# Optimization experiments

Measured on AMD Instinct MI355X. Metric: run time of the kernel, lower is better.

Reference implementation:

```python
import jax, jax.numpy as jnp
import numpy as np
from itertools import combinations_with_replacement

INPUT_DIM = 128
DEGREE = 2

# Static index arrays for degree-2 terms (i<=j), matching
# combinations_with_replacement order.
_pairs = np.array(list(combinations_with_replacement(range(INPUT_DIM), DEGREE)), dtype=np.int32)
I_IDX = jnp.asarray(_pairs[:, 0])  # [d*(d+1)/2]
J_IDX = jnp.asarray(_pairs[:, 1])


def setup_inputs() -> dict:
    key = jax.random.key(0)
    k1, k2, k3 = jax.random.split(key, 3)
    B, D, N = 8192, INPUT_DIM, 512
    num_outputs = D + D * (D + 1) // 2  # 8384
    x = jax.random.normal(k1, (B, D), dtype=jnp.float32)
    weights = jax.random.normal(k2, (N, num_outputs), dtype=jnp.float32)
    bias = jax.random.normal(k3, (N,), dtype=jnp.float32)
    return {"x": x, "weights": weights, "bias": bias}


def reference(x, weights, bias):
    # Polynomial feature expansion: [x, x_i * x_j for i<=j]
    poly = x[:, I_IDX] * x[:, J_IDX]          # [B, d*(d+1)/2]
    feats = jnp.concatenate([x, poly], axis=1)  # [B, num_outputs]
    # (output.unsqueeze(1) * weights.unsqueeze(0)).sum(-1) == feats @ weights.T
    return jnp.einsum('bo,no->bn', feats, weights) + bias
```

## Files before the change

kernel.cpp:

```cpp
#include <hip/hip_runtime.h>
#include <hip/hip_bf16.h>
#include <stdint.h>

#define D_IN   128
#define NPOLY  8256
#define KDIM   8384
#define B_ROWS 8192
#define N_COLS 512

#define WBF_OFF   0
#define WBF_BYTES ((size_t)N_COLS * KDIM * 2)
#define FEA_OFF   WBF_BYTES
#define FEA_BYTES ((size_t)B_ROWS * KDIM * 2)
#define WS_NEED   (FEA_OFF + FEA_BYTES)

typedef __attribute__((ext_vector_type(8))) short    bf16x8_t;
typedef __attribute__((ext_vector_type(8))) float    f32x8_t;
typedef __attribute__((ext_vector_type(4))) float    f32x4_t;
typedef __attribute__((ext_vector_type(4))) uint32_t u32x4_t;

__device__ __forceinline__ uint32_t pk2(float lo, float hi) {
  uint32_t r;
  asm("v_cvt_pk_bf16_f32 %0, %1, %2" : "=v"(r) : "v"(lo), "v"(hi));
  return r;
}

__device__ __forceinline__ void async_load16(void* lds_dst, const void* g_src) {
  __builtin_amdgcn_global_load_lds(
      (const __attribute__((address_space(1))) void*)g_src,
      (__attribute__((address_space(3))) void*)lds_dst,
      16, 0, 0);
}

#define NB_FEAT 4096
#define NB_INIT 4096
#define NB_WCNV 2096
__global__ __launch_bounds__(256) void fused_prep(
    const float* __restrict__ x, const float* __restrict__ w,
    const float* __restrict__ bias, float* __restrict__ out,
    uint16_t* __restrict__ wb, uint16_t* __restrict__ feats) {
  __shared__ float xs[2][D_IN];
  __shared__ __align__(16) uint16_t pr[2][KDIM];
  const int blk = blockIdx.x;
  const int tid = threadIdx.x;

  if (blk < NB_FEAT) {
    const int r0 = blk * 2;
    xs[tid >> 7][tid & 127] = x[(size_t)r0 * D_IN + tid];
    __syncthreads();
    if (tid < 32) {
      int row = tid >> 4, c8 = (tid & 15) * 8;
      u32x4_t o;
#pragma unroll
      for (int h = 0; h < 4; ++h)
        o[h] = pk2(xs[row][c8 + 2 * h], xs[row][c8 + 2 * h + 1]);
      *(u32x4_t*)&pr[row][c8] = o;
    }
    for (int it = 0; it < 5; ++it) {
      int g = tid + it * 256;
      if (g >= NPOLY / 8) break;
      int p0 = 8 * g;
      float t = 66049.0f - 8.0f * (float)p0;
      int i = (int)((257.0f - sqrtf(t)) * 0.5f);
      while (i > 0 && (i * (257 - i)) / 2 > p0) --i;
      while (i < 127 && ((i + 1) * (257 - (i + 1))) / 2 <= p0) ++i;
      int j = i + (p0 - (i * (257 - i)) / 2);
      float xi0 = xs[0][i], xi1 = xs[1][i];
      float q0[8], q1[8];
#pragma unroll
      for (int e = 0; e < 8; ++e) {
        q0[e] = xi0 * xs[0][j];
        q1[e] = xi1 * xs[1][j];
        if (e < 7) {
          if (j == 127) { ++i; j = i; xi0 = xs[0][i]; xi1 = xs[1][i]; }
          else ++j;
        }
      }
      u32x4_t o0, o1;
#pragma unroll
      for (int h = 0; h < 4; ++h) {
        o0[h] = pk2(q0[2 * h], q0[2 * h + 1]);
        o1[h] = pk2(q1[2 * h], q1[2 * h + 1]);
      }
      *(u32x4_t*)&pr[0][D_IN + p0] = o0;
      *(u32x4_t*)&pr[1][D_IN + p0] = o1;
    }
    __syncthreads();
    uint16_t* d0 = feats + (size_t)r0 * KDIM;
    for (int q = tid; q < 2 * (KDIM / 8); q += 256) {
      int row = (q >= KDIM / 8);
      int g = q - (row ? KDIM / 8 : 0);
      *(bf16x8_t*)(d0 + (size_t)row * KDIM + g * 8) =
          *(const bf16x8_t*)&pr[row][g * 8];
    }
  } else if (blk < NB_FEAT + NB_INIT) {
    int idx = (blk - NB_FEAT) * 256 + tid;
    f32x4_t bv = *(const f32x4_t*)(bias + ((idx * 4) & (N_COLS - 1)));
    *(f32x4_t*)(out + (size_t)idx * 4) = bv;
  } else {
    int g = (blk - NB_FEAT - NB_INIT) * 256 + tid;
    f32x8_t v = *(const f32x8_t*)(w + (size_t)g * 8);
    u32x4_t o;
#pragma unroll
    for (int h = 0; h < 4; ++h) o[h] = pk2(v[2 * h], v[2 * h + 1]);
    *(u32x4_t*)(wb + (size_t)g * 8) = o;
  }
}

#define BMT 128
#define BNT 128
#define BKT 64
#define KSTEPS 131
#define KCUT 66

__global__ __launch_bounds__(256, 2) void gemm_poly(
    const uint16_t* __restrict__ A,
    const uint16_t* __restrict__ W,
    float* __restrict__ out) {
  __shared__ __align__(16) uint16_t sA[BMT * BKT];
  __shared__ __align__(16) uint16_t sW[BNT * BKT];

  const int tid  = threadIdx.x;
  const int lane = tid & 63;
  const int wv   = tid >> 6;
  const int wr   = wv >> 1;
  const int wc   = wv & 1;
  const int hi   = lane >> 4;
  const int lr   = lane & 15;

  const int b0 = blockIdx.x * BMT;
  const int n0 = blockIdx.y * BNT;
  const int kt0 = (blockIdx.z == 0) ? 0 : KCUT;
  const int kt1 = (blockIdx.z == 0) ? KCUT : KSTEPS;

  int rowq[4], cbxq[4];
#pragma unroll
  for (int q = 0; q < 4; ++q) {
    int L = q * 4096 + tid * 16;
    int row = L >> 7;
    int cb  = L & 127;
    rowq[q] = row;
    cbxq[q] = cb ^ ((row & 7) << 4);
  }

  int offA[4][2], offW[4][2];
#pragma unroll
  for (int f = 0; f < 4; ++f) {
    int rowA = wr * 64 + f * 16 + lr;
    int rowW = wc * 64 + f * 16 + lr;
#pragma unroll
    for (int kh = 0; kh < 2; ++kh) {
      int kb = kh * 64 + hi * 16;
      offA[f][kh] = rowA * 128 + (kb ^ ((rowA & 7) << 4));
      offW[f][kh] = rowW * 128 + (kb ^ ((rowW & 7) << 4));
    }
  }

  f32x4_t acc[4][4];
#pragma unroll
  for (int mf = 0; mf < 4; ++mf)
#pragma unroll
    for (int nf = 0; nf < 4; ++nf) {
      f32x4_t z = {0.f, 0.f, 0.f, 0.f};
      acc[mf][nf] = z;
    }

  const char* Ab = (const char*)A;
  const char* Wb = (const char*)W;

#define STAGE(kt)                                                              \
  {                                                                            \
    _Pragma("unroll")                                                          \
    for (int q = 0; q < 4; ++q) {                                              \
      const char* srcA =                                                       \
          Ab + ((size_t)(b0 + rowq[q]) * KDIM + (kt) * BKT) * 2 + cbxq[q];     \
      async_load16((char*)sA + q * 4096 + tid * 16, srcA);                     \
    }                                                                          \
    _Pragma("unroll")                                                          \
    for (int q = 0; q < 4; ++q) {                                              \
      const char* srcW =                                                       \
          Wb + ((size_t)(n0 + rowq[q]) * KDIM + (kt) * BKT) * 2 + cbxq[q];     \
      async_load16((char*)sW + q * 4096 + tid * 16, srcW);                     \
    }                                                                          \
  }

  STAGE(kt0);
  for (int kt = kt0; kt < kt1; ++kt) {
    __syncthreads();
    bf16x8_t a[4][2], b[4][2];
#pragma unroll
    for (int mf = 0; mf < 4; ++mf)
#pragma unroll
      for (int kh = 0; kh < 2; ++kh)
        a[mf][kh] = *(const bf16x8_t*)((const char*)sA + offA[mf][kh]);
#pragma unroll
    for (int nf = 0; nf < 4; ++nf)
#pragma unroll
      for (int kh = 0; kh < 2; ++kh)
        b[nf][kh] = *(const bf16x8_t*)((const char*)sW + offW[nf][kh]);
#pragma unroll
    for (int mf = 0; mf < 4; ++mf)
#pragma unroll
      for (int nf = 0; nf < 4; ++nf) {
        acc[mf][nf] = __builtin_amdgcn_mfma_f32_16x16x32_bf16(
            a[mf][0], b[nf][0], acc[mf][nf], 0, 0, 0);
        acc[mf][nf] = __builtin_amdgcn_mfma_f32_16x16x32_bf16(
            a[mf][1], b[nf][1], acc[mf][nf], 0, 0, 0);
      }
    __syncthreads();
    if (kt + 1 < kt1) STAGE(kt + 1);
  }

#pragma unroll
  for (int mf = 0; mf < 4; ++mf) {
    int row = b0 + wr * 64 + mf * 16 + hi * 4;
#pragma unroll
    for (int nf = 0; nf < 4; ++nf) {
      int col = n0 + wc * 64 + nf * 16 + lr;
#pragma unroll
      for (int r = 0; r < 4; ++r) {
        atomicAdd(&out[(size_t)(row + r) * N_COLS + col], acc[mf][nf][r]);
      }
    }
  }
#undef STAGE
}

__global__ void naive_poly(const float* __restrict__ x, const float* __restrict__ w,
                           const float* __restrict__ bias, float* __restrict__ out) {
  size_t o = (size_t)blockIdx.x * 256 + threadIdx.x;
  if (o >= (size_t)B_ROWS * N_COLS) return;
  int n = (int)(o >> 13);
  int b = (int)(o & (B_ROWS - 1));
  const float* xr = x + (size_t)b * D_IN;
  const float* wr = w + (size_t)n * KDIM;
  float acc = bias[n];
  for (int k = 0; k < D_IN; ++k) acc += wr[k] * xr[k];
  int p = D_IN;
  for (int i = 0; i < D_IN; ++i) {
    float xi = xr[i];
    for (int j = i; j < D_IN; ++j) acc += wr[p++] * xi * xr[j];
  }
  out[(size_t)b * N_COLS + n] = acc;
}

extern "C" void kernel_launch(void* const* d_in, const int* in_sizes, int n_in,
                              void* d_out, int out_size, void* d_ws, size_t ws_size,
                              hipStream_t stream) {
  const float* x    = (const float*)d_in[0];
  const float* w    = (const float*)d_in[1];
  const float* bias = (const float*)d_in[2];
  float* out = (float*)d_out;

  if (ws_size < WS_NEED) {
    naive_poly<<<(B_ROWS * N_COLS) / 256, 256, 0, stream>>>(x, w, bias, out);
    return;
  }

  char* ws = (char*)d_ws;
  uint16_t* wb  = (uint16_t*)(ws + WBF_OFF);
  uint16_t* fe  = (uint16_t*)(ws + FEA_OFF);

  fused_prep<<<NB_FEAT + NB_INIT + NB_WCNV, 256, 0, stream>>>(x, w, bias, out, wb, fe);
  gemm_poly<<<dim3(B_ROWS / BMT, N_COLS / BNT, 2), 256, 0, stream>>>(fe, wb, out);
}
```

Baseline: 200.6 us.

## Double-buffer A in LDS, load W straight to registers, remap blocks for XCD locality

The GEMM now double-buffers the A tile in LDS and prefetches the next step's A while computing the current one, using explicit vmcnt waits and raw barriers. The W operand is loaded straight from global memory into registers, ping-ponging between two register sets, so its LDS staging goes away. The launch becomes a 1D grid whose block index is remapped so that blocks on the same XCD share tiles, and MFMA sections run at raised wave priority. The risks are higher register pressure from the register-held W and uncoalesced per-lane global loads for W. A clamp is also added in the feature index computation.

After: 268.3 us. 1.34x slower.

```diff
diff --git a/kernel.cpp b/kernel.cpp
--- a/kernel.cpp
+++ b/kernel.cpp
@@ -62,6 +62,7 @@
       int p0 = 8 * g;
       float t = 66049.0f - 8.0f * (float)p0;
       int i = (int)((257.0f - sqrtf(t)) * 0.5f);
+      if (i < 0) i = 0; if (i > 127) i = 127;
       while (i > 0 && (i * (257 - i)) / 2 > p0) --i;
       while (i < 127 && ((i + 1) * (257 - (i + 1))) / 2 <= p0) ++i;
       int j = i + (p0 - (i * (257 - i)) / 2);
@@ -117,8 +118,7 @@
     const uint16_t* __restrict__ A,
     const uint16_t* __restrict__ W,
     float* __restrict__ out) {
-  __shared__ __align__(16) uint16_t sA[BMT * BKT];
-  __shared__ __align__(16) uint16_t sW[BNT * BKT];
+  __shared__ __align__(16) uint16_t sA[2 * BMT * BKT];
 
   const int tid  = threadIdx.x;
   const int lane = tid & 63;
@@ -128,10 +128,17 @@
   const int hi   = lane >> 4;
   const int lr   = lane & 15;
 
-  const int b0 = blockIdx.x * BMT;
-  const int n0 = blockIdx.y * BNT;
-  const int kt0 = (blockIdx.z == 0) ? 0 : KCUT;
-  const int kt1 = (blockIdx.z == 0) ? KCUT : KSTEPS;
+  const int bid = blockIdx.x;
+  const int lin = (bid & 7) * 64 + (bid >> 3);
+  const int bz  = lin >> 8;
+  const int rem = lin & 255;
+  const int by  = rem >> 6;
+  const int bx  = rem & 63;
+
+  const int b0  = bx * BMT;
+  const int n0  = by * BNT;
+  const int kt0 = (bz == 0) ? 0 : KCUT;
+  const int kt1 = (bz == 0) ? KCUT : KSTEPS;
 
   int rowq[4], cbxq[4];
 #pragma unroll
@@ -143,17 +150,23 @@
     cbxq[q] = cb ^ ((row & 7) << 4);
   }
 
-  int offA[4][2], offW[4][2];
+  int offA[4][2];
 #pragma unroll
   for (int f = 0; f < 4; ++f) {
     int rowA = wr * 64 + f * 16 + lr;
-    int rowW = wc * 64 + f * 16 + lr;
 #pragma unroll
     for (int kh = 0; kh < 2; ++kh) {
       int kb = kh * 64 + hi * 16;
       offA[f][kh] = rowA * 128 + (kb ^ ((rowA & 7) << 4));
-      offW[f][kh] = rowW * 128 + (kb ^ ((rowW & 7) << 4));
-    }
+    }
+  }
+
+  const char* Wb = (const char*)W;
+  const char* wbase[4];
+#pragma unroll
+  for (int nf = 0; nf < 4; ++nf) {
+    int rowW = n0 + wc * 64 + nf * 16 + lr;
+    wbase[nf] = Wb + (size_t)rowW * (KDIM * 2) + hi * 16;
   }
 
   f32x4_t acc[4][4];
@@ -166,49 +179,69 @@
     }
 
   const char* Ab = (const char*)A;
-  const char* Wb = (const char*)W;
-
-#define STAGE(kt)                                                              \
+
+#define STAGE_A(kt, P)                                                         \
   {                                                                            \
     _Pragma("unroll")                                                          \
     for (int q = 0; q < 4; ++q) {                                              \
       const char* srcA =                                                       \
           Ab + ((size_t)(b0 + rowq[q]) * KDIM + (kt) * BKT) * 2 + cbxq[q];     \
-      async_load16((char*)sA + q * 4096 + tid * 16, srcA);                     \
+      async_load16((char*)sA + (P) * 16384 + q * 4096 + tid * 16, srcA);       \
     }                                                                          \
+  }
+
+#define LOADW(DST, kt)                                                         \
+  {                                                                            \
     _Pragma("unroll")                                                          \
-    for (int q = 0; q < 4; ++q) {                                              \
-      const char* srcW =                                                       \
-          Wb + ((size_t)(n0 + rowq[q]) * KDIM + (kt) * BKT) * 2 + cbxq[q];     \
-      async_load16((char*)sW + q * 4096 + tid * 16, srcW);                     \
+    for (int nf = 0; nf < 4; ++nf) {                                           \
+      DST[nf][0] = *(const bf16x8_t*)(wbase[nf] + (kt) * 128);                 \
+      DST[nf][1] = *(const bf16x8_t*)(wbase[nf] + (kt) * 128 + 64);            \
     }                                                                          \
   }
 
-  STAGE(kt0);
-  for (int kt = kt0; kt < kt1; ++kt) {
-    __syncthreads();
-    bf16x8_t a[4][2], b[4][2];
-#pragma unroll
-    for (int mf = 0; mf < 4; ++mf)
-#pragma unroll
-      for (int kh = 0; kh < 2; ++kh)
-        a[mf][kh] = *(const bf16x8_t*)((const char*)sA + offA[mf][kh]);
-#pragma unroll
-    for (int nf = 0; nf < 4; ++nf)
-#pragma unroll
-      for (int kh = 0; kh < 2; ++kh)
-        b[nf][kh] = *(const bf16x8_t*)((const char*)sW + offW[nf][kh]);
-#pragma unroll
-    for (int mf = 0; mf < 4; ++mf)
-#pragma unroll
-      for (int nf = 0; nf < 4; ++nf) {
-        acc[mf][nf] = __builtin_amdgcn_mfma_f32_16x16x32_bf16(
-            a[mf][0], b[nf][0], acc[mf][nf], 0, 0, 0);
-        acc[mf][nf] = __builtin_amdgcn_mfma_f32_16x16x32_bf16(
-            a[mf][1], b[nf][1], acc[mf][nf], 0, 0, 0);
-      }
-    __syncthreads();
-    if (kt + 1 < kt1) STAGE(kt + 1);
+#define ITER(T, BCUR, BNXT, P)                                                 \
+  {                                                                            \
+    const int t_ = (T);                                                        \
+    if (t_ + 1 < kt1) {                                                        \
+      LOADW(BNXT, t_ + 1);                                                     \
+      STAGE_A(t_ + 1, (P) ^ 1);                                                \
+      asm volatile("s_waitcnt vmcnt(12)" ::: "memory");                        \
+    } else {                                                                   \
+      asm volatile("s_waitcnt vmcnt(0)" ::: "memory");                         \
+    }                                                                          \
+    __builtin_amdgcn_s_barrier();                                              \
+    __builtin_amdgcn_sched_barrier(0);                                         \
+    bf16x8_t a_[4][2];                                                         \
+    _Pragma("unroll")                                                          \
+    for (int mf = 0; mf < 4; ++mf) {                                           \
+      a_[mf][0] = *(const bf16x8_t*)((const char*)sA + (P) * 16384 +           \
+                                     offA[mf][0]);                             \
+      a_[mf][1] = *(const bf16x8_t*)((const char*)sA + (P) * 16384 +           \
+                                     offA[mf][1]);                             \
+    }                                                                          \
+    __builtin_amdgcn_s_setprio(1);                                             \
+    _Pragma("unroll")                                                          \
+    for (int mf = 0; mf < 4; ++mf)                                             \
+      _Pragma("unroll")                                                        \
+      for (int nf = 0; nf < 4; ++nf) {                                         \
+        acc[mf][nf] = __builtin_amdgcn_mfma_f32_16x16x32_bf16(                 \
+            a_[mf][0], BCUR[nf][0], acc[mf][nf], 0, 0, 0);                     \
+        acc[mf][nf] = __builtin_amdgcn_mfma_f32_16x16x32_bf16(                 \
+            a_[mf][1], BCUR[nf][1], acc[mf][nf], 0, 0, 0);                     \
+      }                                                                        \
+    __builtin_amdgcn_s_setprio(0);                                             \
+    __builtin_amdgcn_s_barrier();                                              \
+    __builtin_amdgcn_sched_barrier(0);                                         \
+  }
+
+  bf16x8_t bX[4][2], bY[4][2];
+  STAGE_A(kt0, 0);
+  LOADW(bX, kt0);
+
+  const int iters = kt1 - kt0;
+  for (int it = 0; it < iters; it += 2) {
+    ITER(kt0 + it, bX, bY, 0);
+    if (it + 1 < iters) ITER(kt0 + it + 1, bY, bX, 1);
   }
 
 #pragma unroll
@@ -223,7 +256,9 @@
       }
     }
   }
-#undef STAGE
+#undef ITER
+#undef LOADW
+#undef STAGE_A
 }
 
 __global__ void naive_poly(const float* __restrict__ x, const float* __restrict__ w,
@@ -262,5 +297,5 @@
   uint16_t* fe  = (uint16_t*)(ws + FEA_OFF);
 
   fused_prep<<<NB_FEAT + NB_INIT + NB_WCNV, 256, 0, stream>>>(x, w, bias, out, wb, fe);
-  gemm_poly<<<dim3(B_ROWS / BMT, N_COLS / BNT, 2), 256, 0, stream>>>(fe, wb, out);
-}
+  gemm_poly<<<512, 256, 0, stream>>>(fe, wb, out);
+}
```

## Enlarge GEMM M-tile to 256 rows, split K four ways, raise MFMA priority

Applied to the files above, without the earlier changes.

Doubles the block tile along the batch dimension, so each wave computes a 128x64 sub-tile with 32 accumulators. This improves the ratio of weight-tile reuse to LDS traffic. The K dimension is split into four chunks instead of two, which keeps the grid size the same but doubles the atomic adds to the output. The inner loop now loads fragments per k-half and wraps the MFMAs in s_setprio. The larger accumulator array (128 VGPRs) and 48KB of LDS put the two-blocks-per-CU launch bound and register spilling at risk.

After: 208.1 us. 3.7% more time.

```diff
diff --git a/kernel.cpp b/kernel.cpp
--- a/kernel.cpp
+++ b/kernel.cpp
@@ -62,6 +62,7 @@
       int p0 = 8 * g;
       float t = 66049.0f - 8.0f * (float)p0;
       int i = (int)((257.0f - sqrtf(t)) * 0.5f);
+      if (i < 0) i = 0; if (i > 127) i = 127;
       while (i > 0 && (i * (257 - i)) / 2 > p0) --i;
       while (i < 127 && ((i + 1) * (257 - (i + 1))) / 2 <= p0) ++i;
       int j = i + (p0 - (i * (257 - i)) / 2);
@@ -107,11 +108,11 @@
   }
 }
 
-#define BMT 128
+#define BMT 256
 #define BNT 128
 #define BKT 64
 #define KSTEPS 131
-#define KCUT 66
+#define KP     33
 
 __global__ __launch_bounds__(256, 2) void gemm_poly(
     const uint16_t* __restrict__ A,
@@ -130,12 +131,12 @@
 
   const int b0 = blockIdx.x * BMT;
   const int n0 = blockIdx.y * BNT;
-  const int kt0 = (blockIdx.z == 0) ? 0 : KCUT;
-  const int kt1 = (blockIdx.z == 0) ? KCUT : KSTEPS;
-
-  int rowq[4], cbxq[4];
-#pragma unroll
-  for (int q = 0; q < 4; ++q) {
+  const int kt0 = blockIdx.z * KP;
+  int kt1 = kt0 + KP; if (kt1 > KSTEPS) kt1 = KSTEPS;
+
+  int rowq[8], cbxq[8];
+#pragma unroll
+  for (int q = 0; q < 8; ++q) {
     int L = q * 4096 + tid * 16;
     int row = L >> 7;
     int cb  = L & 127;
@@ -143,22 +144,29 @@
     cbxq[q] = cb ^ ((row & 7) << 4);
   }
 
-  int offA[4][2], offW[4][2];
-#pragma unroll
-  for (int f = 0; f < 4; ++f) {
-    int rowA = wr * 64 + f * 16 + lr;
-    int rowW = wc * 64 + f * 16 + lr;
+  int offA[8][2], offW[4][2];
+#pragma unroll
+  for (int f = 0; f < 8; ++f) {
+    int rowA = wr * 128 + f * 16 + lr;
 #pragma unroll
     for (int kh = 0; kh < 2; ++kh) {
       int kb = kh * 64 + hi * 16;
       offA[f][kh] = rowA * 128 + (kb ^ ((rowA & 7) << 4));
+    }
+  }
+#pragma unroll
+  for (int f = 0; f < 4; ++f) {
+    int rowW = wc * 64 + f * 16 + lr;
+#pragma unroll
+    for (int kh = 0; kh < 2; ++kh) {
+      int kb = kh * 64 + hi * 16;
       offW[f][kh] = rowW * 128 + (kb ^ ((rowW & 7) << 4));
     }
   }
 
-  f32x4_t acc[4][4];
-#pragma unroll
-  for (int mf = 0; mf < 4; ++mf)
+  f32x4_t acc[8][4];
+#pragma unroll
+  for (int mf = 0; mf < 8; ++mf)
 #pragma unroll
     for (int nf = 0; nf < 4; ++nf) {
       f32x4_t z = {0.f, 0.f, 0.f, 0.f};
@@ -171,7 +179,7 @@
 #define STAGE(kt)                                                              \
   {                                                                            \
     _Pragma("unroll")                                                          \
-    for (int q = 0; q < 4; ++q) {                                              \
+    for (int q = 0; q < 8; ++q) {                                              \
       const char* srcA =                                                       \
           Ab + ((size_t)(b0 + rowq[q]) * KDIM + (kt) * BKT) * 2 + cbxq[q];     \
       async_load16((char*)sA + q * 4096 + tid * 16, srcA);                     \
@@ -187,33 +195,31 @@
   STAGE(kt0);
   for (int kt = kt0; kt < kt1; ++kt) {
     __syncthreads();
-    bf16x8_t a[4][2], b[4][2];
-#pragma unroll
-    for (int mf = 0; mf < 4; ++mf)
-#pragma unroll
-      for (int kh = 0; kh < 2; ++kh)
-        a[mf][kh] = *(const bf16x8_t*)((const char*)sA + offA[mf][kh]);
-#pragma unroll
-    for (int nf = 0; nf < 4; ++nf)
-#pragma unroll
-      for (int kh = 0; kh < 2; ++kh)
-        b[nf][kh] = *(const bf16x8_t*)((const char*)sW + offW[nf][kh]);
-#pragma unroll
-    for (int mf = 0; mf < 4; ++mf)
-#pragma unroll
-      for (int nf = 0; nf < 4; ++nf) {
-        acc[mf][nf] = __builtin_amdgcn_mfma_f32_16x16x32_bf16(
-            a[mf][0], b[nf][0], acc[mf][nf], 0, 0, 0);
-        acc[mf][nf] = __builtin_amdgcn_mfma_f32_16x16x32_bf16(
-            a[mf][1], b[nf][1], acc[mf][nf], 0, 0, 0);
-      }
+#pragma unroll
+    for (int kh = 0; kh < 2; ++kh) {
+      bf16x8_t a[8], b[4];
+#pragma unroll
+      for (int mf = 0; mf < 8; ++mf)
+        a[mf] = *(const bf16x8_t*)((const char*)sA + offA[mf][kh]);
+#pragma unroll
+      for (int nf = 0; nf < 4; ++nf)
+        b[nf] = *(const bf16x8_t*)((const char*)sW + offW[nf][kh]);
+      __builtin_amdgcn_s_setprio(1);
+#pragma unroll
+      for (int mf = 0; mf < 8; ++mf)
+#pragma unroll
+        for (int nf = 0; nf < 4; ++nf)
+          acc[mf][nf] = __builtin_amdgcn_mfma_f32_16x16x32_bf16(
+              a[mf], b[nf], acc[mf][nf], 0, 0, 0);
+      __builtin_amdgcn_s_setprio(0);
+    }
     __syncthreads();
     if (kt + 1 < kt1) STAGE(kt + 1);
   }
 
 #pragma unroll
-  for (int mf = 0; mf < 4; ++mf) {
-    int row = b0 + wr * 64 + mf * 16 + hi * 4;
+  for (int mf = 0; mf < 8; ++mf) {
+    int row = b0 + wr * 128 + mf * 16 + hi * 4;
 #pragma unroll
     for (int nf = 0; nf < 4; ++nf) {
       int col = n0 + wc * 64 + nf * 16 + lr;
@@ -262,5 +268,5 @@
   uint16_t* fe  = (uint16_t*)(ws + FEA_OFF);
 
   fused_prep<<<NB_FEAT + NB_INIT + NB_WCNV, 256, 0, stream>>>(x, w, bias, out, wb, fe);
-  gemm_poly<<<dim3(B_ROWS / BMT, N_COLS / BNT, 2), 256, 0, stream>>>(fe, wb, out);
-}
+  gemm_poly<<<dim3(B_ROWS / BMT, N_COLS / BNT, 4), 256, 0, stream>>>(fe, wb, out);
+}
```
